# Kernel tuning notes

Measured on AMD Instinct MI355X. Metric: run time of the kernel, lower is better.

The kernel has to match this reference:

```python
import jax, jax.numpy as jnp
import numpy as np

N_QUBITS = 16
DEPTH = 4
BATCH = 512

# Convention: wire 0 is the most-significant bit of the state index (PennyLane default).

def _rx(t):
    # t: scalar or (B,) real angle -> (2,2) or (B,2,2) complex RX matrix
    h = 0.5 * t
    c = jnp.cos(h).astype(jnp.complex64)
    s = (-1j * jnp.sin(h)).astype(jnp.complex64)
    return jnp.stack([jnp.stack([c, s], -1), jnp.stack([s, c], -1)], -2)

def _ry(t):
    h = 0.5 * t
    c = jnp.cos(h).astype(jnp.complex64)
    s = jnp.sin(h).astype(jnp.complex64)
    return jnp.stack([jnp.stack([c, -s], -1), jnp.stack([s, c], -1)], -2)

def _rz(t):
    e = jnp.exp(-0.5j * t.astype(jnp.complex64))  # diag(e^{-it/2}, e^{+it/2})
    z = jnp.zeros_like(e)
    return jnp.stack([jnp.stack([e, z], -1), jnp.stack([z, jnp.conj(e)], -1)], -2)

def _apply_1q(state, U, q, n):
    # state: (B, 2^n); U: (2,2) shared or (B,2,2) per-batch
    B = state.shape[0]
    L, R = 2 ** q, 2 ** (n - q - 1)
    s = state.reshape(B, L, 2, R)
    if U.ndim == 2:
        s = jnp.einsum('ij,bljr->blir', U, s)
    else:
        s = jnp.einsum('bij,bljr->blir', U, s)
    return s.reshape(B, -1)

def _apply_cnot(state, c, t, n):
    # flips target bit t where control bit c == 1
    B = state.shape[0]
    a, b = min(c, t), max(c, t)
    s = state.reshape(B, 2 ** a, 2, 2 ** (b - a - 1), 2, 2 ** (n - b - 1))
    if c < t:
        # control axis=2, target axis=4
        s1 = s[:, :, 1]                      # (B, 2^a, mid, 2, rest)
        flipped = s1[:, :, :, ::-1, :]
        s = jnp.stack([s[:, :, 0], flipped], axis=2)
    else:
        # control axis=4, target axis=2
        s1 = s[:, :, :, :, 1, :]             # (B, 2^a, 2, mid, rest)
        flipped = s1[:, :, ::-1]
        s = jnp.stack([s[:, :, :, :, 0, :], flipped], axis=4)
    return s.reshape(B, -1)

def _circuit(x, params):
    B, n = x.shape
    depth = params.shape[0]
    state = jnp.zeros((B, 2 ** n), jnp.complex64).at[:, 0].set(1.0)
    # data encoding: batched RX per wire
    for i in range(n):
        state = _apply_1q(state, _rx(x[:, i]), i, n)
    for layer in range(depth):
        for i in range(n):
            # circuit applies RZ then RX then RY -> fuse into one 2x2 matrix
            U = _ry(params[layer, i, 2]) @ _rx(params[layer, i, 1]) @ _rz(params[layer, i, 0])
            state = _apply_1q(state, U, i, n)
        for i in range(n - 1):
            state = _apply_cnot(state, i, i + 1, n)
        state = _apply_cnot(state, n - 1, 0, n)
    # <Z_i> = P(bit_i = 0) - P(bit_i = 1)
    probs = state.real ** 2 + state.imag ** 2
    expz = []
    for i in range(n):
        p = probs.reshape(B, 2 ** i, 2, 2 ** (n - i - 1))
        expz.append(p[:, :, 0].sum((1, 2)) - p[:, :, 1].sum((1, 2)))
    return jnp.stack(expz, axis=1)  # (B, n_qubits)


def setup_inputs() -> dict:
    key = jax.random.key(0)
    k1, k2 = jax.random.split(key)
    x = jax.random.normal(k1, (BATCH, N_QUBITS), dtype=jnp.float32)
    params = jax.random.normal(k2, (DEPTH, N_QUBITS, 3), dtype=jnp.float32)
    return {"x": x, "params": params}


def reference(x, params):
    return _circuit(x, params)
```

## Files before the change

### kernel.cpp

```cpp
#include <hip/hip_runtime.h>


#define NQ 16
#define TPB 256

typedef float __attribute__((ext_vector_type(2))) f2;

__device__ __forceinline__ f2 f2s(float s) { return (f2){s, s}; }

__device__ __forceinline__ f2 cmulpk(f2 a, f2 b) {
    f2 bs = { -b.y, b.x };
    f2 r = f2s(a.x) * b;
    return __builtin_elementwise_fma(f2s(a.y), bs, r);
}

__device__ __forceinline__ void computeU(const float* params, int layer, int q, f2* U) {
    const float* p = params + (layer*NQ + q)*3;
    float s0, c0, s1, c1, s2, c2;
    sincosf(0.5f*p[0], &s0, &c0);
    sincosf(0.5f*p[1], &s1, &c1);
    sincosf(0.5f*p[2], &s2, &c2);
    f2 m00 = { c1*c0, -c1*s0};
    f2 m01 = { s1*s0, -s1*c0};
    f2 m10 = {-s1*s0, -s1*c0};
    f2 m11 = { c1*c0,  c1*s0};
    U[0] = c2*m00 - s2*m10;
    U[1] = c2*m01 - s2*m11;
    U[2] = s2*m00 + c2*m10;
    U[3] = s2*m01 + c2*m11;
}

template<int MASK>
__device__ __forceinline__ void gate32(f2* A, f2 u00, f2 u01, f2 u10, f2 u11) {
    #pragma unroll
    for (int a = 0; a < 32; ++a) {
        if (!(a & MASK)) {
            f2 x = A[a], y = A[a | MASK];
            f2 xs = { -x.y, x.x };
            f2 ys = { -y.y, y.x };
            f2 nx = f2s(u00.x) * x;
            nx = __builtin_elementwise_fma(f2s(u00.y), xs, nx);
            nx = __builtin_elementwise_fma(f2s(u01.x), y,  nx);
            nx = __builtin_elementwise_fma(f2s(u01.y), ys, nx);
            f2 ny = f2s(u10.x) * x;
            ny = __builtin_elementwise_fma(f2s(u10.y), xs, ny);
            ny = __builtin_elementwise_fma(f2s(u11.x), y,  ny);
            ny = __builtin_elementwise_fma(f2s(u11.y), ys, ny);
            A[a] = nx; A[a | MASK] = ny;
        }
    }
}

__device__ __forceinline__ constexpr int permB(int ad) {
    return (ad & 1)
         | ((((ad >> 1) ^ (ad >> 2)) & 1) << 1)
         | ((((ad >> 2) ^ (ad >> 3)) & 1) << 2)
         | ((((ad >> 3) ^ (ad >> 4)) & 1) << 3)
         | ((((ad >> 4) ^  ad      ) & 1) << 4);
}

__device__ __forceinline__ void b_gates_and_store(
    f2* A, f2* S, const f2 (*Ush)[4], int t, int fixb, f2* base)
{
    gate32<1> (A, Ush[0][0],  Ush[0][1],  Ush[0][2],  Ush[0][3]);
    gate32<2> (A, Ush[1][0],  Ush[1][1],  Ush[1][2],  Ush[1][3]);
    gate32<4> (A, Ush[2][0],  Ush[2][1],  Ush[2][2],  Ush[2][3]);
    gate32<8> (A, Ush[3][0],  Ush[3][1],  Ush[3][2],  Ush[3][3]);
    gate32<16>(A, Ush[4][0],  Ush[4][1],  Ush[4][2],  Ush[4][3]);

    #pragma unroll
    for (int h = 0; h < 2; ++h) {
        __syncthreads();
        #pragma unroll
        for (int c = 0; c < 8; ++c) {
            int slot = ((t << 1) | (c << 9)) ^ (((t >> 4) & 7) << 1);
            f2 a0 = A[h*16 + 2*c], a1 = A[h*16 + 2*c + 1];
            *(float4*)&S[slot] = make_float4(a0.x, a0.y, a1.x, a1.y);
        }
        __syncthreads();
        #pragma unroll
        for (int rr = 0; rr < 16; ++rr) {
            int jj = (t & 1) | (rr << 1) | (((t >> 1) & 15) << 5) | (((t >> 5) & 7) << 9);
            A[h*16 + rr] = S[jj ^ (((t >> 1) & 7) << 1)];
        }
    }

    gate32<1>(A, Ush[5][0], Ush[5][1], Ush[5][2], Ush[5][3]);
    gate32<2>(A, Ush[6][0], Ush[6][1], Ush[6][2], Ush[6][3]);
    gate32<4>(A, Ush[7][0], Ush[7][1], Ush[7][2], Ush[7][3]);
    gate32<8>(A, Ush[8][0], Ush[8][1], Ush[8][2], Ush[8][3]);

    #pragma unroll
    for (int h = 0; h < 2; ++h) {
        __syncthreads();
        #pragma unroll
        for (int rr = 0; rr < 16; ++rr) {
            int jj = (t & 1) | (rr << 1) | (((t >> 1) & 15) << 5) | (((t >> 5) & 7) << 9);
            S[jj ^ (((t >> 1) & 7) << 1)] = A[h*16 + rr];
        }
        __syncthreads();
        #pragma unroll
        for (int rr = 0; rr < 16; ++rr) {
            int jj = (t & 31) | (rr << 5) | (((t >> 5) & 7) << 9);
            A[h*16 + rr] = S[jj ^ ((rr & 7) << 1)];
        }
    }

    gate32<1>(A, Ush[9][0],  Ush[9][1],  Ush[9][2],  Ush[9][3]);
    gate32<2>(A, Ush[10][0], Ush[10][1], Ush[10][2], Ush[10][3]);
    gate32<4>(A, Ush[11][0], Ush[11][1], Ush[11][2], Ush[11][3]);
    gate32<8>(A, Ush[12][0], Ush[12][1], Ush[12][2], Ush[12][3]);

    #pragma unroll
    for (int h = 0; h < 2; ++h) {
        #pragma unroll
        for (int rr = 0; rr < 16; ++rr) {
            int d = (t & 31) | (rr << 5) | (((t >> 5) & 7) << 9) | (h << 12);
            int m = (d & 511) | (fixb << 9) | (((d >> 9) & 1) << 12) | ((d >> 10) << 13);
            base[m] = A[h*16 + rr];
        }
    }
}

__global__ __launch_bounds__(TPB, 4) void qc_B1_gen(
    const float* __restrict__ x, const float* __restrict__ params,
    f2* __restrict__ st)
{
    __shared__ __align__(16) f2 S[4096];
    __shared__ f2 Ush[13][4];
    __shared__ f2 V[16][2];

    const int t    = threadIdx.x;
    const int b    = blockIdx.x >> 3;
    const int fixb = blockIdx.x & 7;
    f2* base = st + ((size_t)b << NQ);

    if (t < 16) {
        f2 U[4];
        computeU(params, 0, t, U);
        float s, c;
        sincosf(0.5f * x[b*NQ + t], &s, &c);
        V[15 - t][0] = (f2){U[0].x*c + U[1].y*s, U[0].y*c - U[1].x*s};
        V[15 - t][1] = (f2){U[2].x*c + U[3].y*s, U[2].y*c - U[3].x*s};
    } else if (t < 29) {
        int tt = t - 16;
        int qb = (tt == 0) ? 12 : (tt == 1) ? 0 : (tt < 5) ? (17 - tt) : (16 - tt);
        computeU(params, 1, qb, Ush[tt]);
    }
    __syncthreads();

    const int f0 = fixb & 1, f1 = (fixb >> 1) & 1, f2b = (fixb >> 2) & 1;
    const int t0 = t & 1,  t7 = (t >> 7) & 1;

    f2 pre = V[4][(t ^ (t >> 1)) & 1];
    #pragma unroll
    for (int bb = 5; bb <= 10; ++bb)
        pre = cmulpk(pre, V[bb][((t >> (bb - 4)) ^ (t >> (bb - 3))) & 1]);
    pre = cmulpk(pre, V[11][t7 ^ f0]);
    pre = cmulpk(pre, V[12][f0 ^ f1]);
    pre = cmulpk(pre, V[13][f1 ^ f2b]);

    f2 P0 = cmulpk(pre, V[3][t0]);
    f2 P1 = cmulpk(pre, V[3][1 ^ t0]);
    f2 Q[4];
    Q[0] = cmulpk(P0, V[2][0]); Q[1] = cmulpk(P1, V[2][0]);
    Q[2] = cmulpk(P0, V[2][1]); Q[3] = cmulpk(P1, V[2][1]);
    f2 Rr[4];
    Rr[0] = cmulpk(V[0][0], V[1][0]); Rr[1] = cmulpk(V[0][1], V[1][0]);
    Rr[2] = cmulpk(V[0][0], V[1][1]); Rr[3] = cmulpk(V[0][1], V[1][1]);
    f2 G0 = cmulpk(V[15][0], V[14][f2b]);
    f2 G1 = cmulpk(V[15][1], V[14][1 ^ f2b]);
    f2 TT[8];
    #pragma unroll
    for (int e = 0; e < 4; ++e) {
        TT[2*e]     = cmulpk(G0, Rr[e]);
        TT[2*e + 1] = cmulpk(G1, Rr[e]);
    }

    f2 A[32];
    #pragma unroll
    for (int a = 0; a < 32; ++a) {
        const int a0 = a & 1;
        const int e1 = ((a >> 1) ^ (a >> 2)) & 1;
        const int e2 = ((a >> 2) ^ (a >> 3)) & 1;
        const int e3 = ((a >> 3) ^ (a >> 4)) & 1;
        const int e4 = ((a >> 4) ^  a      ) & 1;
        A[a] = cmulpk(Q[a0 + 2*e4], TT[e1 + 2*e2 + 4*e3]);
    }

    b_gates_and_store(A, S, Ush, t, fixb, base);
}

__global__ __launch_bounds__(TPB, 4) void qc_B_heavy(
    const float* __restrict__ params, f2* __restrict__ st, int lm)
{
    __shared__ __align__(16) f2 S[4096];
    __shared__ f2 Ush[13][4];

    const int t    = threadIdx.x;
    const int b    = blockIdx.x >> 3;
    const int fixb = blockIdx.x & 7;
    f2* base = st + ((size_t)b << NQ);

    if (t < 13) {
        int qb = (t == 0) ? 12 : (t == 1) ? 0 : (t < 5) ? (17 - t) : (16 - t);
        computeU(params, lm, qb, Ush[t]);
    }

    f2 R[32];
    #pragma unroll
    for (int k = 0; k < 16; ++k) {
        int j = 2*(t + 256*k);
        int m = (j & 511) | (fixb << 9) | (((j >> 9) & 1) << 12) | ((j >> 10) << 13);
        float4 v = *(const float4*)(base + m);
        R[2*k]   = (f2){v.x, v.y};
        R[2*k+1] = (f2){v.z, v.w};
    }
    f2 A[32];
    #pragma unroll
    for (int a = 0; a < 32; ++a) A[a] = R[permB(a)];
    __syncthreads();

    b_gates_and_store(A, S, Ush, t, fixb, base);
}

__global__ __launch_bounds__(TPB, 4) void qc_A_lite(
    const float* __restrict__ params, f2* __restrict__ st, int layer)
{
    __shared__ __align__(16) f2 S[4096];
    __shared__ f2 Ush[3][4];
    const int t    = threadIdx.x;
    const int b    = blockIdx.x >> 3;
    const int fix3 = blockIdx.x & 7;
    f2* base = st + ((size_t)b << NQ) + (fix3 << 13);

    if (t < 3) computeU(params, layer, 3 - t, Ush[t]);

    f2 A[32];
    const float4* src = (const float4*)base;
    #pragma unroll
    for (int k = 0; k < 16; ++k) {
        float4 v = src[t + 256*k];
        A[2*k]   = (f2){v.x, v.y};
        A[2*k+1] = (f2){v.z, v.w};
    }
    __syncthreads();

    gate32<2>(A, Ush[0][0], Ush[0][1], Ush[0][2], Ush[0][3]);
    gate32<4>(A, Ush[1][0], Ush[1][1], Ush[1][2], Ush[1][3]);
    gate32<8>(A, Ush[2][0], Ush[2][1], Ush[2][2], Ush[2][3]);

    float4* dst = (float4*)base;
    #pragma unroll
    for (int h = 0; h < 2; ++h) {
        __syncthreads();
        #pragma unroll
        for (int c = 0; c < 8; ++c) {
            int slot = ((t << 1) | (c << 9)) ^ (((t >> 4) & 7) << 1);
            f2 a0 = A[h*16 + 2*c], a1 = A[h*16 + 2*c + 1];
            *(float4*)&S[slot] = make_float4(a0.x, a0.y, a1.x, a1.y);
        }
        __syncthreads();
        #pragma unroll
        for (int k = 0; k < 8; ++k) {
            int d  = 2*(t + 256*k);
            int i0 = d ^ (d >> 1) ^ (h << 11);
            int i1 = (d+1) ^ ((d+1) >> 1) ^ (h << 11);
            f2 a0 = S[i0 ^ (((i0 >> 5) & 7) << 1)];
            f2 a1 = S[i1 ^ (((i1 >> 5) & 7) << 1)];
            dst[(t + 256*k) | (h << 11)] = make_float4(a0.x, a0.y, a1.x, a1.y);
        }
    }
}

__global__ __launch_bounds__(TPB) void qc_A_final(
    const float* __restrict__ params, const f2* __restrict__ st,
    float* __restrict__ out)
{
    __shared__ f2 Ush[3][4];
    const int t    = threadIdx.x;
    const int b    = blockIdx.x >> 3;
    const int fix3 = blockIdx.x & 7;
    const f2* base = st + ((size_t)b << NQ) + (fix3 << 13);

    if (t < 3) computeU(params, 3, 3 - t, Ush[t]);

    f2 A[32];
    const float4* src = (const float4*)base;
    #pragma unroll
    for (int k = 0; k < 16; ++k) {
        float4 v = src[t + 256*k];
        A[2*k]   = (f2){v.x, v.y};
        A[2*k+1] = (f2){v.z, v.w};
    }
    __syncthreads();

    gate32<2>(A, Ush[0][0], Ush[0][1], Ush[0][2], Ush[0][3]);
    gate32<4>(A, Ush[1][0], Ush[1][1], Ush[1][2], Ush[1][3]);
    gate32<8>(A, Ush[2][0], Ush[2][1], Ush[2][2], Ush[2][3]);

    float m1 = 0.f, m2 = 0.f, m3 = 0.f, m4 = 0.f, m5 = 0.f;
    #pragma unroll
    for (int a = 0; a < 32; ++a) {
        float p = A[a].x*A[a].x + A[a].y*A[a].y;
        m1 += (__popc(a & 0x1E) & 1) ? -p : p;
        m2 += (__popc(a & 0x1F) & 1) ? -p : p;
        m3 += (__popc(a & 0x1C) & 1) ? -p : p;
        m4 += (__popc(a & 0x18) & 1) ? -p : p;
        m5 += (__popc(a & 0x0F) & 1) ? -p : p;
    }
    const int pt = __popc(t) & 1;
    const int pf = __popc(fix3) & 1;
    float acc[NQ];
    acc[0] = ((pt ^ pf) & 1) ? -m5 : m5;
    acc[1] = m4;
    acc[2] = m3;
    acc[3] = m1;
    #pragma unroll
    for (int q = 4; q <= 11; ++q) {
        int s = __popc(t >> (11 - q)) & 1;
        acc[q] = s ? -m1 : m1;
    }
    acc[12] = pt ? -m2 : m2;
    acc[13] = ((pt ^ (fix3 >> 2)) & 1) ? -m2 : m2;
    acc[14] = ((pt ^ __popc(fix3 >> 1)) & 1) ? -m2 : m2;
    acc[15] = ((pt ^ pf) & 1) ? -m2 : m2;

    #pragma unroll
    for (int q = 0; q < NQ; ++q) {
        float v = acc[q];
        v += __shfl_down(v, 32, 64);
        v += __shfl_down(v, 16, 64);
        v += __shfl_down(v,  8, 64);
        v += __shfl_down(v,  4, 64);
        v += __shfl_down(v,  2, 64);
        v += __shfl_down(v,  1, 64);
        acc[q] = v;
    }
    if ((t & 63) == 0) {
        #pragma unroll
        for (int q = 0; q < NQ; ++q)
            atomicAdd(&out[b*NQ + q], acc[q]);
    }
}

extern "C" void kernel_launch(void* const* d_in, const int* in_sizes, int n_in,
                              void* d_out, int out_size, void* d_ws, size_t ws_size,
                              hipStream_t stream)
{
    (void)in_sizes; (void)n_in; (void)ws_size;
    const float* x      = (const float*)d_in[0];
    const float* params = (const float*)d_in[1];
    float* out = (float*)d_out;
    f2* st = (f2*)d_ws;

    hipMemsetAsync(d_out, 0, (size_t)out_size * sizeof(float), stream);
    qc_B1_gen <<<dim3(512*8), dim3(TPB), 0, stream>>>(x, params, st);
    qc_A_lite <<<dim3(512*8), dim3(TPB), 0, stream>>>(params, st, 1);
    qc_B_heavy<<<dim3(512*8), dim3(TPB), 0, stream>>>(params, st, 2);
    qc_A_lite <<<dim3(512*8), dim3(TPB), 0, stream>>>(params, st, 2);
    qc_B_heavy<<<dim3(512*8), dim3(TPB), 0, stream>>>(params, st, 3);
    qc_A_final<<<dim3(512*8), dim3(TPB), 0, stream>>>(params, st, out);
}
```

Baseline: 597.9 us.

## Fold next-layer low-qubit gates into A pass and drop final A kernel

The A-pass kernel now applies the following layer's gates on qubits 1-3 after its permuting shared-memory reshuffle, so the work the old final A kernel did moves earlier in the schedule. The last B pass becomes a fused B_final that runs the gates and computes the Z expectation values directly, with sign bookkeeping recomputed for the new index layout. This removes one full read of the 512x65536 complex state from global memory and one kernel launch. The cost is more register pressure in the A kernel and a more intricate parity mapping in the final reduction.

After: 753.1 us. +26.0%, slower.

```diff
diff --git a/kernel.cpp b/kernel.cpp
--- a/kernel.cpp
+++ b/kernel.cpp
@@ -30,10 +30,10 @@
     U[3] = s2*m01 + c2*m11;
 }
 
-template<int MASK>
-__device__ __forceinline__ void gate32(f2* A, f2 u00, f2 u01, f2 u10, f2 u11) {
-    #pragma unroll
-    for (int a = 0; a < 32; ++a) {
+template<int MASK, int N>
+__device__ __forceinline__ void gateN(f2* A, f2 u00, f2 u01, f2 u10, f2 u11) {
+    #pragma unroll
+    for (int a = 0; a < N; ++a) {
         if (!(a & MASK)) {
             f2 x = A[a], y = A[a | MASK];
             f2 xs = { -x.y, x.x };
@@ -50,6 +50,8 @@
         }
     }
 }
+template<int MASK> __device__ __forceinline__ void gate32(f2* A, f2 a, f2 b, f2 c, f2 d) { gateN<MASK,32>(A,a,b,c,d); }
+template<int MASK> __device__ __forceinline__ void gate16(f2* A, f2 a, f2 b, f2 c, f2 d) { gateN<MASK,16>(A,a,b,c,d); }
 
 __device__ __forceinline__ constexpr int permB(int ad) {
     return (ad & 1)
@@ -59,8 +61,8 @@
          | ((((ad >> 4) ^  ad      ) & 1) << 4);
 }
 
-__device__ __forceinline__ void b_gates_and_store(
-    f2* A, f2* S, const f2 (*Ush)[4], int t, int fixb, f2* base)
+__device__ __forceinline__ void b_gates_core(
+    f2* A, f2* S, const f2 (*Ush)[4], int t)
 {
     gate32<1> (A, Ush[0][0],  Ush[0][1],  Ush[0][2],  Ush[0][3]);
     gate32<2> (A, Ush[1][0],  Ush[1][1],  Ush[1][2],  Ush[1][3]);
@@ -110,7 +112,11 @@
     gate32<2>(A, Ush[10][0], Ush[10][1], Ush[10][2], Ush[10][3]);
     gate32<4>(A, Ush[11][0], Ush[11][1], Ush[11][2], Ush[11][3]);
     gate32<8>(A, Ush[12][0], Ush[12][1], Ush[12][2], Ush[12][3]);
-
+}
+
+__device__ __forceinline__ void b_store(
+    const f2* A, int t, int fixb, f2* base)
+{
     #pragma unroll
     for (int h = 0; h < 2; ++h) {
         #pragma unroll
@@ -188,7 +194,8 @@
         A[a] = cmulpk(Q[a0 + 2*e4], TT[e1 + 2*e2 + 4*e3]);
     }
 
-    b_gates_and_store(A, S, Ush, t, fixb, base);
+    b_gates_core(A, S, Ush, t);
+    b_store(A, t, fixb, base);
 }
 
 __global__ __launch_bounds__(TPB, 4) void qc_B_heavy(
@@ -221,20 +228,22 @@
     for (int a = 0; a < 32; ++a) A[a] = R[permB(a)];
     __syncthreads();
 
-    b_gates_and_store(A, S, Ush, t, fixb, base);
-}
-
-__global__ __launch_bounds__(TPB, 4) void qc_A_lite(
-    const float* __restrict__ params, f2* __restrict__ st, int layer)
+    b_gates_core(A, S, Ush, t);
+    b_store(A, t, fixb, base);
+}
+
+__global__ __launch_bounds__(TPB, 4) void qc_A_mid(
+    const float* __restrict__ params, f2* __restrict__ st, int preL, int postL)
 {
     __shared__ __align__(16) f2 S[4096];
-    __shared__ f2 Ush[3][4];
+    __shared__ f2 Up[3][4], Uq[3][4];
     const int t    = threadIdx.x;
     const int b    = blockIdx.x >> 3;
     const int fix3 = blockIdx.x & 7;
     f2* base = st + ((size_t)b << NQ) + (fix3 << 13);
 
-    if (t < 3) computeU(params, layer, 3 - t, Ush[t]);
+    if (t < 3 && preL >= 0) computeU(params, preL, 3 - t, Up[t]);
+    if (t >= 4 && t < 7)    computeU(params, postL, 3 - (t - 4), Uq[t - 4]);
 
     f2 A[32];
     const float4* src = (const float4*)base;
@@ -246,9 +255,11 @@
     }
     __syncthreads();
 
-    gate32<2>(A, Ush[0][0], Ush[0][1], Ush[0][2], Ush[0][3]);
-    gate32<4>(A, Ush[1][0], Ush[1][1], Ush[1][2], Ush[1][3]);
-    gate32<8>(A, Ush[2][0], Ush[2][1], Ush[2][2], Ush[2][3]);
+    if (preL >= 0) {
+        gate32<2>(A, Up[0][0], Up[0][1], Up[0][2], Up[0][3]);
+        gate32<4>(A, Up[1][0], Up[1][1], Up[1][2], Up[1][3]);
+        gate32<8>(A, Up[2][0], Up[2][1], Up[2][2], Up[2][3]);
+    }
 
     float4* dst = (float4*)base;
     #pragma unroll
@@ -261,70 +272,97 @@
             *(float4*)&S[slot] = make_float4(a0.x, a0.y, a1.x, a1.y);
         }
         __syncthreads();
+        f2 Bv[16];
         #pragma unroll
         for (int k = 0; k < 8; ++k) {
             int d  = 2*(t + 256*k);
             int i0 = d ^ (d >> 1) ^ (h << 11);
             int i1 = (d+1) ^ ((d+1) >> 1) ^ (h << 11);
-            f2 a0 = S[i0 ^ (((i0 >> 5) & 7) << 1)];
-            f2 a1 = S[i1 ^ (((i1 >> 5) & 7) << 1)];
+            Bv[2*k]     = S[i0 ^ (((i0 >> 5) & 7) << 1)];
+            Bv[2*k + 1] = S[i1 ^ (((i1 >> 5) & 7) << 1)];
+        }
+        gate16<2>(Bv, Uq[0][0], Uq[0][1], Uq[0][2], Uq[0][3]);
+        gate16<4>(Bv, Uq[1][0], Uq[1][1], Uq[1][2], Uq[1][3]);
+        gate16<8>(Bv, Uq[2][0], Uq[2][1], Uq[2][2], Uq[2][3]);
+        #pragma unroll
+        for (int k = 0; k < 8; ++k) {
+            f2 a0 = Bv[2*k], a1 = Bv[2*k + 1];
             dst[(t + 256*k) | (h << 11)] = make_float4(a0.x, a0.y, a1.x, a1.y);
         }
     }
 }
 
-__global__ __launch_bounds__(TPB) void qc_A_final(
+__global__ __launch_bounds__(TPB, 4) void qc_B_final(
     const float* __restrict__ params, const f2* __restrict__ st,
     float* __restrict__ out)
 {
-    __shared__ f2 Ush[3][4];
+    __shared__ __align__(16) f2 S[4096];
+    __shared__ f2 Ush[13][4];
+
     const int t    = threadIdx.x;
     const int b    = blockIdx.x >> 3;
-    const int fix3 = blockIdx.x & 7;
-    const f2* base = st + ((size_t)b << NQ) + (fix3 << 13);
-
-    if (t < 3) computeU(params, 3, 3 - t, Ush[t]);
-
+    const int fixb = blockIdx.x & 7;
+    const f2* base = st + ((size_t)b << NQ);
+
+    if (t < 13) {
+        int qb = (t == 0) ? 12 : (t == 1) ? 0 : (t < 5) ? (17 - t) : (16 - t);
+        computeU(params, 3, qb, Ush[t]);
+    }
+
+    f2 R[32];
+    #pragma unroll
+    for (int k = 0; k < 16; ++k) {
+        int j = 2*(t + 256*k);
+        int m = (j & 511) | (fixb << 9) | (((j >> 9) & 1) << 12) | ((j >> 10) << 13);
+        float4 v = *(const float4*)(base + m);
+        R[2*k]   = (f2){v.x, v.y};
+        R[2*k+1] = (f2){v.z, v.w};
+    }
     f2 A[32];
-    const float4* src = (const float4*)base;
-    #pragma unroll
-    for (int k = 0; k < 16; ++k) {
-        float4 v = src[t + 256*k];
-        A[2*k]   = (f2){v.x, v.y};
-        A[2*k+1] = (f2){v.z, v.w};
-    }
+    #pragma unroll
+    for (int a = 0; a < 32; ++a) A[a] = R[permB(a)];
     __syncthreads();
 
-    gate32<2>(A, Ush[0][0], Ush[0][1], Ush[0][2], Ush[0][3]);
-    gate32<4>(A, Ush[1][0], Ush[1][1], Ush[1][2], Ush[1][3]);
-    gate32<8>(A, Ush[2][0], Ush[2][1], Ush[2][2], Ush[2][3]);
-
-    float m1 = 0.f, m2 = 0.f, m3 = 0.f, m4 = 0.f, m5 = 0.f;
-    #pragma unroll
-    for (int a = 0; a < 32; ++a) {
-        float p = A[a].x*A[a].x + A[a].y*A[a].y;
-        m1 += (__popc(a & 0x1E) & 1) ? -p : p;
-        m2 += (__popc(a & 0x1F) & 1) ? -p : p;
-        m3 += (__popc(a & 0x1C) & 1) ? -p : p;
-        m4 += (__popc(a & 0x18) & 1) ? -p : p;
-        m5 += (__popc(a & 0x0F) & 1) ? -p : p;
-    }
-    const int pt = __popc(t) & 1;
-    const int pf = __popc(fix3) & 1;
+    b_gates_core(A, S, Ush, t);
+
+    float M0 = 0.f, M1 = 0.f, M2 = 0.f, M3 = 0.f, M4 = 0.f, M5 = 0.f;
+    #pragma unroll
+    for (int h = 0; h < 2; ++h) {
+        #pragma unroll
+        for (int rr = 0; rr < 16; ++rr) {
+            f2 v = A[h*16 + rr];
+            float p = v.x*v.x + v.y*v.y;
+            M0 += p;
+            M1 += (__popc(rr)      & 1) ? -p : p;
+            M2 += (__popc(rr >> 1) & 1) ? -p : p;
+            M3 += (__popc(rr >> 2) & 1) ? -p : p;
+            M4 += (rr >> 3)             ? -p : p;
+            M5 += ((__popc(rr) ^ h) & 1) ? -p : p;
+        }
+    }
+
+    const int pf   = __popc(fixb) & 1;
+    const int t5b  = (t >> 5) & 1, t6b = (t >> 6) & 1, t7b = (t >> 7) & 1;
+    const int pt04 = __popc(t & 31) & 1;
+    const int bs   = pf ^ t5b;
+
     float acc[NQ];
-    acc[0] = ((pt ^ pf) & 1) ? -m5 : m5;
-    acc[1] = m4;
-    acc[2] = m3;
-    acc[3] = m1;
-    #pragma unroll
-    for (int q = 4; q <= 11; ++q) {
-        int s = __popc(t >> (11 - q)) & 1;
-        acc[q] = s ? -m1 : m1;
-    }
-    acc[12] = pt ? -m2 : m2;
-    acc[13] = ((pt ^ (fix3 >> 2)) & 1) ? -m2 : m2;
-    acc[14] = ((pt ^ __popc(fix3 >> 1)) & 1) ? -m2 : m2;
-    acc[15] = ((pt ^ pf) & 1) ? -m2 : m2;
+    acc[0]  = ((t6b ^ t7b ^ pt04 ^ pf) & 1) ? -M5 : M5;
+    acc[1]  = (((fixb >> 2) ^ t5b) & 1)      ? -M0 : M0;
+    acc[2]  = ((__popc(fixb >> 1) ^ t5b) & 1)? -M0 : M0;
+    acc[3]  = (bs & 1)                        ? -M0 : M0;
+    acc[4]  = (bs & 1)                        ? -M4 : M4;
+    acc[5]  = (bs & 1)                        ? -M3 : M3;
+    acc[6]  = (bs & 1)                        ? -M2 : M2;
+    acc[7]  = (bs & 1)                        ? -M1 : M1;
+    acc[8]  = ((((t >> 4) & 1) ^ bs) & 1)     ? -M1 : M1;
+    acc[9]  = ((__popc((t >> 3) & 3)  ^ bs) & 1) ? -M1 : M1;
+    acc[10] = ((__popc((t >> 2) & 7)  ^ bs) & 1) ? -M1 : M1;
+    acc[11] = ((__popc((t >> 1) & 15) ^ bs) & 1) ? -M1 : M1;
+    acc[12] = ((pt04 ^ bs) & 1)               ? -M1 : M1;
+    acc[13] = ((pt04 ^ bs) & 1)               ? -M5 : M5;
+    acc[14] = ((t7b ^ pt04 ^ bs) & 1)         ? -M5 : M5;
+    acc[15] = ((t6b ^ t7b ^ pt04 ^ bs) & 1)   ? -M5 : M5;
 
     #pragma unroll
     for (int q = 0; q < NQ; ++q) {
@@ -356,9 +394,8 @@
 
     hipMemsetAsync(d_out, 0, (size_t)out_size * sizeof(float), stream);
     qc_B1_gen <<<dim3(512*8), dim3(TPB), 0, stream>>>(x, params, st);
-    qc_A_lite <<<dim3(512*8), dim3(TPB), 0, stream>>>(params, st, 1);
+    qc_A_mid  <<<dim3(512*8), dim3(TPB), 0, stream>>>(params, st, 1, 2);
     qc_B_heavy<<<dim3(512*8), dim3(TPB), 0, stream>>>(params, st, 2);
-    qc_A_lite <<<dim3(512*8), dim3(TPB), 0, stream>>>(params, st, 2);
-    qc_B_heavy<<<dim3(512*8), dim3(TPB), 0, stream>>>(params, st, 3);
-    qc_A_final<<<dim3(512*8), dim3(TPB), 0, stream>>>(params, st, out);
-}
+    qc_A_mid  <<<dim3(512*8), dim3(TPB), 0, stream>>>(params, st, -1, 3);
+    qc_B_final<<<dim3(512*8), dim3(TPB), 0, stream>>>(params, st, out);
+}
```
